# Kernel tuning notes

Measured on AMD Instinct MI355X. Metric: run time of the kernel, lower is better.

The kernel has to match this reference:

```python
import jax, jax.numpy as jnp
import numpy as np

B, S, D = 4, 4096, 1024
E, I = 8, 2048
CAPACITY = 2
K = max(1, int(S / E * CAPACITY))  # tokens per expert per batch element


def setup_inputs() -> dict:
    key = jax.random.key(0)
    k1, k2, k3, k4, k5 = jax.random.split(key, 5)
    x = jax.random.normal(k1, (B, S, D), dtype=jnp.float32)
    gate_w = jax.random.normal(k2, (D, E), dtype=jnp.float32) * 0.006
    Wg = jax.random.normal(k3, (E, D, I), dtype=jnp.float32) * 0.02
    Wu = jax.random.normal(k4, (E, D, I), dtype=jnp.float32) * 0.02
    Wd = jax.random.normal(k5, (E, I, D), dtype=jnp.float32) * 0.02
    return {"x": x, "gate_w": gate_w, "Wg": Wg, "Wu": Wu, "Wd": Wd}


def reference(x, gate_w, Wg, Wu, Wd):
    # Router: softmax over experts per token, then per-expert top-k tokens.
    logits = jnp.einsum('bsd,de->bse', x, gate_w)          # [B,S,E]
    affinity = jax.nn.softmax(logits, axis=-1)
    affinity_T = jnp.transpose(affinity, (0, 2, 1))        # [B,E,S]
    gating, index = jax.lax.top_k(affinity_T, K)           # [B,E,K]

    # Gather selected tokens for all experts at once: [B,E,K,D]
    b_idx = jnp.arange(x.shape[0])[:, None, None]
    x_sel = x[b_idx, index]

    # Per-expert SwiGLU MLP (grouped GEMMs over the expert axis).
    g = jnp.einsum('bekd,edi->beki', x_sel, Wg)
    u = jnp.einsum('bekd,edi->beki', x_sel, Wu)
    h = jax.nn.silu(g) * u
    out = jnp.einsum('beki,eid->bekd', h, Wd)              # [B,E,K,D]

    # Weighted scatter-add combine back to token positions.
    contrib = out * gating[..., None]
    x_out = jnp.zeros_like(x).at[b_idx, index].add(contrib)
    return x_out
```

## Files before the change

kernel.cpp:

```cpp
#include <hip/hip_runtime.h>

#define B_ 4
#define S_ 4096
#define D_ 1024
#define E_ 8
#define I_ 2048
#define K_ 1024

typedef __attribute__((ext_vector_type(8))) short short8;
typedef __attribute__((ext_vector_type(4))) float f32x4;

__device__ __forceinline__ short f2bf(float f) {
  union { float f; unsigned u; } v; v.f = f;
  unsigned r = v.u + 0x7FFFu + ((v.u >> 16) & 1u);
  return (short)(r >> 16);
}

__device__ __forceinline__ void gload16(const void* g, void* l) {
  __builtin_amdgcn_global_load_lds((const __attribute__((address_space(1))) unsigned int*)g,
                                   (__attribute__((address_space(3))) unsigned int*)l, 16, 0, 0);
}

__device__ __forceinline__ short8 rdswz(const short* ls, int row, int cb) {
  int byte = (row << 7) + (cb ^ ((row & 7) << 4));
  return *reinterpret_cast<const short8*>(reinterpret_cast<const char*>(ls) + byte);
}

__global__ __launch_bounds__(256) void router_kernel(const float* __restrict__ x,
                                                     const float* __restrict__ gw,
                                                     double* __restrict__ affD) {
  int wave = threadIdx.x >> 6, lane = threadIdx.x & 63;
  int tok = blockIdx.x * 4 + wave;
  int b = tok >> 12, s = tok & (S_ - 1);
  const float* xr = x + (size_t)tok * D_;
  double acc[E_];
#pragma unroll
  for (int e = 0; e < E_; ++e) acc[e] = 0.0;
#pragma unroll 4
  for (int r = 0; r < 16; ++r) {
    int d = r * 64 + lane;
    float xv = xr[d];
    const float4* g4 = reinterpret_cast<const float4*>(gw + (size_t)d * E_);
    float4 g0 = g4[0], g1 = g4[1];
    acc[0] += (double)xv * g0.x; acc[1] += (double)xv * g0.y;
    acc[2] += (double)xv * g0.z; acc[3] += (double)xv * g0.w;
    acc[4] += (double)xv * g1.x; acc[5] += (double)xv * g1.y;
    acc[6] += (double)xv * g1.z; acc[7] += (double)xv * g1.w;
  }
#pragma unroll
  for (int off = 32; off > 0; off >>= 1) {
#pragma unroll
    for (int e = 0; e < E_; ++e) acc[e] += __shfl_xor(acc[e], off, 64);
  }
  double m = acc[0];
#pragma unroll
  for (int e = 1; e < E_; ++e) m = acc[e] > m ? acc[e] : m;
  double den = 0.0, ex[E_];
#pragma unroll
  for (int e = 0; e < E_; ++e) { ex[e] = exp(acc[e] - m); den += ex[e]; }
  if (lane < E_)
    affD[((size_t)b * E_ + lane) * S_ + s] = ex[lane] / den;
}

__global__ __launch_bounds__(1024) void topk_select_kernel(const double* __restrict__ affD,
                                                           int* __restrict__ idxArr,
                                                           float* __restrict__ gateArr) {
  __shared__ unsigned hist[256];
  __shared__ unsigned s_digit;
  __shared__ int s_rem;
  __shared__ unsigned s_cnt;
  int be = blockIdx.x, tid = threadIdx.x;
  const double* a = affD + (size_t)be * S_;
  unsigned long long key[4];
  bool active[4];
#pragma unroll
  for (int c = 0; c < 4; ++c) {
    int i = tid + c * 1024;
    unsigned long long kb = (unsigned long long)__double_as_longlong(a[i]);
    key[c] = (kb & ~0xFFFULL) | (unsigned long long)(4095 - i);
    active[c] = true;
  }
  int remk = K_;
  unsigned long long prefix = 0;
  for (int pass = 0; pass < 8; ++pass) {
    int shift = 56 - pass * 8;
    if (tid < 256) hist[tid] = 0;
    __syncthreads();
#pragma unroll
    for (int c = 0; c < 4; ++c)
      if (active[c]) atomicAdd(&hist[(unsigned)((key[c] >> shift) & 0xFF)], 1u);
    __syncthreads();
    if (tid == 0) {
      unsigned cum = 0; int d = 255;
      for (; d > 0; --d) {
        unsigned h = hist[d];
        if (cum + h >= (unsigned)remk) break;
        cum += h;
      }
      s_digit = (unsigned)d;
      s_rem = remk - (int)cum;
    }
    __syncthreads();
    unsigned dg = s_digit; remk = s_rem;
    prefix |= ((unsigned long long)dg) << shift;
#pragma unroll
    for (int c = 0; c < 4; ++c)
      active[c] = active[c] && (((key[c] >> shift) & 0xFF) == dg);
    __syncthreads();
  }
  if (tid == 0) s_cnt = 0;
  __syncthreads();
#pragma unroll
  for (int c = 0; c < 4; ++c) {
    if (key[c] >= prefix) {
      unsigned slot = atomicAdd(&s_cnt, 1u);
      int i = 4095 - (int)(key[c] & 0xFFF);
      idxArr[(size_t)be * K_ + slot] = i;
      gateArr[(size_t)be * K_ + slot] = (float)a[i];
    }
  }
}

__global__ __launch_bounds__(256) void transpose_cvt_kernel(const float* __restrict__ in,
                                                            unsigned short* __restrict__ out,
                                                            int M, int N) {
  __shared__ float t[64][65];
  int e = blockIdx.y;
  int ntn = N >> 6;
  int tm = (blockIdx.x / ntn) << 6;
  int tn = (blockIdx.x % ntn) << 6;
  const float* src = in + (size_t)e * M * N;
  unsigned short* dst = out + (size_t)e * M * N;
  int tid = threadIdx.x;
#pragma unroll
  for (int it = 0; it < 4; ++it) {
    int f = it * 256 + tid;
    int r = f >> 4, c4 = (f & 15) << 2;
    float4 v = *reinterpret_cast<const float4*>(&src[(size_t)(tm + r) * N + tn + c4]);
    t[c4][r] = v.x; t[c4 + 1][r] = v.y; t[c4 + 2][r] = v.z; t[c4 + 3][r] = v.w;
  }
  __syncthreads();
#pragma unroll
  for (int it = 0; it < 4; ++it) {
    int f = it * 256 + tid;
    int rr = f >> 4, c4 = (f & 15) << 2;
    short4 o;
    o.x = f2bf(t[rr][c4]); o.y = f2bf(t[rr][c4 + 1]);
    o.z = f2bf(t[rr][c4 + 2]); o.w = f2bf(t[rr][c4 + 3]);
    *reinterpret_cast<short4*>(&dst[(size_t)(tn + rr) * M + tm + c4]) = o;
  }
}

__global__ __launch_bounds__(256) void gather_cvt_kernel(const float* __restrict__ x,
                                                         const int* __restrict__ idxArr,
                                                         unsigned short* __restrict__ Xsel) {
  int row = blockIdx.x * 4 + (threadIdx.x >> 6);
  int lane = threadIdx.x & 63;
  int b = row >> 13;
  int tok = idxArr[row];
  const float* src = x + ((size_t)b * S_ + tok) * D_;
  unsigned short* dst = Xsel + (size_t)row * D_;
#pragma unroll
  for (int it = 0; it < 4; ++it) {
    int d = it * 256 + lane * 4;
    float4 v = *reinterpret_cast<const float4*>(src + d);
    short4 o;
    o.x = f2bf(v.x); o.y = f2bf(v.y); o.z = f2bf(v.z); o.w = f2bf(v.w);
    *reinterpret_cast<short4*>(dst + d) = o;
  }
}

__global__ __launch_bounds__(256, 2) void mlp1_kernel(
    const unsigned short* __restrict__ Xsel, const unsigned short* __restrict__ WgT,
    const unsigned short* __restrict__ WuT, unsigned short* __restrict__ H,
    int Ic, int i0) {
  const int Nt = Ic >> 7;
  int nwg = gridDim.x;
  int bid = (blockIdx.x & 7) * (nwg >> 3) + (blockIdx.x >> 3);
  int nt = bid % Nt; bid /= Nt;
  int mt = bid & 7; bid >>= 3;
  int be = bid;
  int e = be & 7;

  __shared__ short lsA[128 * 64];
  __shared__ short lsBg[128 * 64];
  __shared__ short lsBu[128 * 64];

  int tid = threadIdx.x, w = tid >> 6, lane = tid & 63;
  int wm = w >> 1, wn = w & 1;
  int lr = lane & 15, lg = lane >> 4;

  int srow = lane >> 3;
  int scol = ((lane & 7) ^ srow) << 4;

  const char* pa = (const char*)(Xsel + ((size_t)be * K_ + mt * 128) * D_);
  const char* pg = (const char*)(WgT + (size_t)e * I_ * D_ + (size_t)(i0 + nt * 128) * D_);
  const char* pu = (const char*)(WuT + (size_t)e * I_ * D_ + (size_t)(i0 + nt * 128) * D_);

  f32x4 accg[4][4], accu[4][4];
#pragma unroll
  for (int i = 0; i < 4; ++i)
#pragma unroll
    for (int j = 0; j < 4; ++j) {
      accg[i][j] = (f32x4){0.f, 0.f, 0.f, 0.f};
      accu[i][j] = (f32x4){0.f, 0.f, 0.f, 0.f};
    }

  for (int k0 = 0; k0 < D_; k0 += 64) {
#pragma unroll
    for (int c = 0; c < 4; ++c) {
      int chunk = c * 4 + w;
      int row = chunk * 8 + srow;
      size_t go = (size_t)row * (D_ * 2) + (size_t)k0 * 2 + scol;
      gload16(pa + go, (char*)lsA + chunk * 1024);
      gload16(pg + go, (char*)lsBg + chunk * 1024);
      gload16(pu + go, (char*)lsBu + chunk * 1024);
    }
    __syncthreads();
#pragma unroll
    for (int fk = 0; fk < 2; ++fk) {
      int cb = fk * 64 + lg * 16;
      short8 af[4], bgf[4], buf[4];
#pragma unroll
      for (int fm = 0; fm < 4; ++fm)
        af[fm] = rdswz(lsA, wm * 64 + fm * 16 + lr, cb);
#pragma unroll
      for (int fn = 0; fn < 4; ++fn) {
        bgf[fn] = rdswz(lsBg, wn * 64 + fn * 16 + lr, cb);
        buf[fn] = rdswz(lsBu, wn * 64 + fn * 16 + lr, cb);
      }
#pragma unroll
      for (int fm = 0; fm < 4; ++fm)
#pragma unroll
        for (int fn = 0; fn < 4; ++fn) {
          accg[fm][fn] = __builtin_amdgcn_mfma_f32_16x16x32_bf16(af[fm], bgf[fn], accg[fm][fn], 0, 0, 0);
          accu[fm][fn] = __builtin_amdgcn_mfma_f32_16x16x32_bf16(af[fm], buf[fn], accu[fm][fn], 0, 0, 0);
        }
    }
    __syncthreads();
  }
  unsigned short* Hbe = H + (size_t)be * K_ * Ic;
#pragma unroll
  for (int fm = 0; fm < 4; ++fm)
#pragma unroll
    for (int fn = 0; fn < 4; ++fn) {
#pragma unroll
      for (int j = 0; j < 4; ++j) {
        float g = accg[fm][fn][j], u = accu[fm][fn][j];
        float h = g / (1.f + __expf(-g)) * u;
        int row = wm * 64 + fm * 16 + lg * 4 + j;
        int col = wn * 64 + fn * 16 + lr;
        Hbe[(size_t)(mt * 128 + row) * Ic + nt * 128 + col] = (unsigned short)f2bf(h);
      }
    }
}

__global__ __launch_bounds__(256, 2) void mlp2_kernel(
    const unsigned short* __restrict__ H, const unsigned short* __restrict__ WdT,
    const int* __restrict__ idxArr, const float* __restrict__ gateArr,
    float* __restrict__ out, int Ic, int i0) {
  int nwg = gridDim.x;
  int bid = (blockIdx.x & 7) * (nwg >> 3) + (blockIdx.x >> 3);
  int nt = bid & 7; bid >>= 3;
  int mt = bid & 7; bid >>= 3;
  int be = bid;
  int b = be >> 3, e = be & 7;

  __shared__ short lsA[128 * 64];
  __shared__ short lsB[128 * 64];
  __shared__ int sTok[128];
  __shared__ float sGate[128];

  int tid = threadIdx.x;
  if (tid < 128) {
    sTok[tid] = idxArr[(size_t)be * K_ + mt * 128 + tid];
    sGate[tid] = gateArr[(size_t)be * K_ + mt * 128 + tid];
  }

  const char* pa = (const char*)(H + ((size_t)be * K_ + mt * 128) * Ic);
  const char* pb = (const char*)(WdT + (size_t)e * D_ * I_ + (size_t)(nt * 128) * I_ + i0);

  int w = tid >> 6, lane = tid & 63;
  int wm = w >> 1, wn = w & 1;
  int lr = lane & 15, lg = lane >> 4;

  int srow = lane >> 3;
  int scol = ((lane & 7) ^ srow) << 4;

  f32x4 acc[4][4];
#pragma unroll
  for (int i = 0; i < 4; ++i)
#pragma unroll
    for (int j = 0; j < 4; ++j) acc[i][j] = (f32x4){0.f, 0.f, 0.f, 0.f};

  for (int k0 = 0; k0 < Ic; k0 += 64) {
#pragma unroll
    for (int c = 0; c < 4; ++c) {
      int chunk = c * 4 + w;
      int row = chunk * 8 + srow;
      gload16(pa + (size_t)row * (Ic * 2) + (size_t)k0 * 2 + scol, (char*)lsA + chunk * 1024);
      gload16(pb + (size_t)row * (I_ * 2) + (size_t)k0 * 2 + scol, (char*)lsB + chunk * 1024);
    }
    __syncthreads();
#pragma unroll
    for (int fk = 0; fk < 2; ++fk) {
      int cb = fk * 64 + lg * 16;
      short8 af[4], bf[4];
#pragma unroll
      for (int fm = 0; fm < 4; ++fm)
        af[fm] = rdswz(lsA, wm * 64 + fm * 16 + lr, cb);
#pragma unroll
      for (int fn = 0; fn < 4; ++fn)
        bf[fn] = rdswz(lsB, wn * 64 + fn * 16 + lr, cb);
#pragma unroll
      for (int fm = 0; fm < 4; ++fm)
#pragma unroll
        for (int fn = 0; fn < 4; ++fn)
          acc[fm][fn] = __builtin_amdgcn_mfma_f32_16x16x32_bf16(af[fm], bf[fn], acc[fm][fn], 0, 0, 0);
    }
    __syncthreads();
  }
#pragma unroll
  for (int fm = 0; fm < 4; ++fm)
#pragma unroll
    for (int fn = 0; fn < 4; ++fn) {
#pragma unroll
      for (int j = 0; j < 4; ++j) {
        int row = wm * 64 + fm * 16 + lg * 4 + j;
        int col = nt * 128 + wn * 64 + fn * 16 + lr;
        float v = acc[fm][fn][j] * sGate[row];
        atomicAdd(&out[((size_t)b * S_ + sTok[row]) * D_ + col], v);
      }
    }
}

extern "C" void kernel_launch(void* const* d_in, const int* in_sizes, int n_in,
                              void* d_out, int out_size, void* d_ws, size_t ws_size,
                              hipStream_t stream) {
  const float* x  = (const float*)d_in[0];
  const float* gw = (const float*)d_in[1];
  const float* Wg = (const float*)d_in[2];
  const float* Wu = (const float*)d_in[3];
  const float* Wd = (const float*)d_in[4];
  float* out = (float*)d_out;
  char* ws = (char*)d_ws;

  size_t off = 0;
  double* affD = (double*)(ws + off); off += (size_t)B_ * E_ * S_ * sizeof(double);
  int* idxArr = (int*)(ws + off);     off += (size_t)B_ * E_ * K_ * sizeof(int);
  float* gateArr = (float*)(ws + off); off += (size_t)B_ * E_ * K_ * sizeof(float);
  off = (off + 255) & ~(size_t)255;
  unsigned short* WgT = (unsigned short*)(ws + off); off += (size_t)E_ * D_ * I_ * 2;
  unsigned short* WuT = (unsigned short*)(ws + off); off += (size_t)E_ * D_ * I_ * 2;
  unsigned short* WdT = (unsigned short*)(ws + off); off += (size_t)E_ * D_ * I_ * 2;
  unsigned short* Xsel = (unsigned short*)(ws + off); off += (size_t)B_ * E_ * K_ * D_ * 2;
  off = (off + 255) & ~(size_t)255;
  unsigned short* H = (unsigned short*)(ws + off);
  size_t rem = (ws_size > off) ? (ws_size - off) : 0;

  int Ic = 128;
  for (int c = I_; c >= 128; c >>= 1) {
    if ((size_t)B_ * E_ * K_ * (size_t)c * 2 <= rem) { Ic = c; break; }
  }

  hipMemsetAsync(d_out, 0, (size_t)out_size * sizeof(float), stream);
  router_kernel<<<B_ * S_ / 4, 256, 0, stream>>>(x, gw, affD);
  topk_select_kernel<<<B_ * E_, 1024, 0, stream>>>(affD, idxArr, gateArr);
  transpose_cvt_kernel<<<dim3((D_ / 64) * (I_ / 64), E_), 256, 0, stream>>>(Wg, WgT, D_, I_);
  transpose_cvt_kernel<<<dim3((D_ / 64) * (I_ / 64), E_), 256, 0, stream>>>(Wu, WuT, D_, I_);
  transpose_cvt_kernel<<<dim3((I_ / 64) * (D_ / 64), E_), 256, 0, stream>>>(Wd, WdT, I_, D_);
  gather_cvt_kernel<<<B_ * E_ * K_ / 4, 256, 0, stream>>>(x, idxArr, Xsel);
  for (int i0 = 0; i0 < I_; i0 += Ic) {
    mlp1_kernel<<<B_ * E_ * 8 * (Ic / 128), 256, 0, stream>>>(Xsel, WgT, WuT, H, Ic, i0);
    mlp2_kernel<<<B_ * E_ * 8 * 8, 256, 0, stream>>>(H, WdT, idxArr, gateArr, out, Ic, i0);
  }
}
```

Baseline: 792.6 us.

## Enlarge MLP GEMM tiles to 256x256 with double-buffered LDS pipeline

Both grouped GEMM kernels move to 512-thread blocks with 256x256 (mlp2) or 256x128 interleaved gate/up (mlp1) output tiles. Each kernel now uses 128-wide K stages with double-buffered LDS, prefetching stage t+2 while computing stage t, and raises MFMA priority with setprio. mlp1 packs gate and up rows into a single B tile so one MFMA loop covers both, and SwiGLU is applied across paired fragments. The aim is more data reuse per loaded byte and overlap of global loads with compute, at the cost of larger LDS and register use, which may lower occupancy.

```diff
diff --git a/kernel.cpp b/kernel.cpp
--- a/kernel.cpp
+++ b/kernel.cpp
@@ -170,7 +170,7 @@
   }
 }
 
-__global__ __launch_bounds__(256, 2) void mlp1_kernel(
+__global__ __launch_bounds__(512, 2) void mlp1_kernel(
     const unsigned short* __restrict__ Xsel, const unsigned short* __restrict__ WgT,
     const unsigned short* __restrict__ WuT, unsigned short* __restrict__ H,
     int Ic, int i0) {
@@ -178,156 +178,203 @@
   int nwg = gridDim.x;
   int bid = (blockIdx.x & 7) * (nwg >> 3) + (blockIdx.x >> 3);
   int nt = bid % Nt; bid /= Nt;
-  int mt = bid & 7; bid >>= 3;
+  int mt = bid & 3; bid >>= 2;
   int be = bid;
   int e = be & 7;
 
-  __shared__ short lsA[128 * 64];
-  __shared__ short lsBg[128 * 64];
-  __shared__ short lsBu[128 * 64];
+  __shared__ short lsA[2][256 * 64];
+  __shared__ short lsB[2][256 * 64];
 
   int tid = threadIdx.x, w = tid >> 6, lane = tid & 63;
-  int wm = w >> 1, wn = w & 1;
+  int wm = w >> 2, wn = w & 3;
   int lr = lane & 15, lg = lane >> 4;
-
   int srow = lane >> 3;
   int scol = ((lane & 7) ^ srow) << 4;
 
-  const char* pa = (const char*)(Xsel + ((size_t)be * K_ + mt * 128) * D_);
-  const char* pg = (const char*)(WgT + (size_t)e * I_ * D_ + (size_t)(i0 + nt * 128) * D_);
-  const char* pu = (const char*)(WuT + (size_t)e * I_ * D_ + (size_t)(i0 + nt * 128) * D_);
-
-  f32x4 accg[4][4], accu[4][4];
-#pragma unroll
-  for (int i = 0; i < 4; ++i)
-#pragma unroll
-    for (int j = 0; j < 4; ++j) {
-      accg[i][j] = (f32x4){0.f, 0.f, 0.f, 0.f};
-      accu[i][j] = (f32x4){0.f, 0.f, 0.f, 0.f};
-    }
-
-  for (int k0 = 0; k0 < D_; k0 += 64) {
-#pragma unroll
-    for (int c = 0; c < 4; ++c) {
-      int chunk = c * 4 + w;
-      int row = chunk * 8 + srow;
-      size_t go = (size_t)row * (D_ * 2) + (size_t)k0 * 2 + scol;
-      gload16(pa + go, (char*)lsA + chunk * 1024);
-      gload16(pg + go, (char*)lsBg + chunk * 1024);
-      gload16(pu + go, (char*)lsBu + chunk * 1024);
-    }
-    __syncthreads();
-#pragma unroll
-    for (int fk = 0; fk < 2; ++fk) {
-      int cb = fk * 64 + lg * 16;
-      short8 af[4], bgf[4], buf[4];
-#pragma unroll
-      for (int fm = 0; fm < 4; ++fm)
-        af[fm] = rdswz(lsA, wm * 64 + fm * 16 + lr, cb);
-#pragma unroll
-      for (int fn = 0; fn < 4; ++fn) {
-        bgf[fn] = rdswz(lsBg, wn * 64 + fn * 16 + lr, cb);
-        buf[fn] = rdswz(lsBu, wn * 64 + fn * 16 + lr, cb);
+  const char* pa = (const char*)(Xsel + ((size_t)be * K_ + mt * 256) * D_);
+  const char* pg = (const char*)(WgT + ((size_t)e * I_ + i0 + nt * 128) * D_);
+  const char* pu = (const char*)(WuT + ((size_t)e * I_ + i0 + nt * 128) * D_);
+
+  auto STAGE = [&](int t) {
+    int buf = t & 1;
+    int kb = t * 128;
+#pragma unroll
+    for (int ch = 0; ch < 4; ++ch) {
+      int rb = ch * 64 + w * 8;
+      int r = rb + srow;
+      gload16(pa + (size_t)r * 2048 + kb + scol, (char*)(&lsA[buf][0]) + rb * 128);
+      int hu = (r >> 4) & 1;
+      int iloc = ((r >> 5) << 4) + (r & 15);
+      const char* pb = hu ? pu : pg;
+      gload16(pb + (size_t)iloc * 2048 + kb + scol, (char*)(&lsB[buf][0]) + rb * 128);
+    }
+  };
+
+  f32x4 acc[8][4];
+#pragma unroll
+  for (int i = 0; i < 8; ++i)
+#pragma unroll
+    for (int j = 0; j < 4; ++j) acc[i][j] = (f32x4){0.f, 0.f, 0.f, 0.f};
+
+  const int NT = 16;
+  STAGE(0);
+  STAGE(1);
+  asm volatile("s_waitcnt vmcnt(8) lgkmcnt(0)" ::: "memory");
+  __builtin_amdgcn_s_barrier();
+
+  for (int t = 0; t < NT; ++t) {
+    const short* A = &lsA[t & 1][0];
+    const short* Bt = &lsB[t & 1][0];
+    short8 af0[8], bf0[4];
+#pragma unroll
+    for (int fm = 0; fm < 8; ++fm) af0[fm] = rdswz(A, wm * 128 + fm * 16 + lr, lg * 16);
+#pragma unroll
+    for (int fn = 0; fn < 4; ++fn) bf0[fn] = rdswz(Bt, wn * 64 + fn * 16 + lr, lg * 16);
+    __builtin_amdgcn_s_setprio(1);
+#pragma unroll
+    for (int fm = 0; fm < 8; ++fm)
+#pragma unroll
+      for (int fn = 0; fn < 4; ++fn)
+        acc[fm][fn] = __builtin_amdgcn_mfma_f32_16x16x32_bf16(af0[fm], bf0[fn], acc[fm][fn], 0, 0, 0);
+    __builtin_amdgcn_s_setprio(0);
+    short8 af1[8], bf1[4];
+#pragma unroll
+    for (int fm = 0; fm < 8; ++fm) af1[fm] = rdswz(A, wm * 128 + fm * 16 + lr, 64 + lg * 16);
+#pragma unroll
+    for (int fn = 0; fn < 4; ++fn) bf1[fn] = rdswz(Bt, wn * 64 + fn * 16 + lr, 64 + lg * 16);
+    asm volatile("s_waitcnt lgkmcnt(0)" ::: "memory");
+    __builtin_amdgcn_s_barrier();
+    if (t + 2 < NT) STAGE(t + 2);
+    __builtin_amdgcn_s_setprio(1);
+#pragma unroll
+    for (int fm = 0; fm < 8; ++fm)
+#pragma unroll
+      for (int fn = 0; fn < 4; ++fn)
+        acc[fm][fn] = __builtin_amdgcn_mfma_f32_16x16x32_bf16(af1[fm], bf1[fn], acc[fm][fn], 0, 0, 0);
+    __builtin_amdgcn_s_setprio(0);
+    if (t + 1 < NT) {
+      if (t + 2 < NT) asm volatile("s_waitcnt vmcnt(8)" ::: "memory");
+      else            asm volatile("s_waitcnt vmcnt(0)" ::: "memory");
+      __builtin_amdgcn_s_barrier();
+    }
+  }
+
+  unsigned short* Hbe = H + (size_t)be * K_ * Ic;
+#pragma unroll
+  for (int fm = 0; fm < 8; ++fm)
+#pragma unroll
+    for (int q = 0; q < 2; ++q)
+#pragma unroll
+      for (int j = 0; j < 4; ++j) {
+        float g = acc[fm][2 * q][j], u = acc[fm][2 * q + 1][j];
+        float h = g / (1.f + __expf(-g)) * u;
+        int row = mt * 256 + wm * 128 + fm * 16 + lg * 4 + j;
+        int col = nt * 128 + (wn * 2 + q) * 16 + lr;
+        Hbe[(size_t)row * Ic + col] = (unsigned short)f2bf(h);
       }
-#pragma unroll
-      for (int fm = 0; fm < 4; ++fm)
-#pragma unroll
-        for (int fn = 0; fn < 4; ++fn) {
-          accg[fm][fn] = __builtin_amdgcn_mfma_f32_16x16x32_bf16(af[fm], bgf[fn], accg[fm][fn], 0, 0, 0);
-          accu[fm][fn] = __builtin_amdgcn_mfma_f32_16x16x32_bf16(af[fm], buf[fn], accu[fm][fn], 0, 0, 0);
-        }
-    }
-    __syncthreads();
-  }
-  unsigned short* Hbe = H + (size_t)be * K_ * Ic;
-#pragma unroll
-  for (int fm = 0; fm < 4; ++fm)
-#pragma unroll
-    for (int fn = 0; fn < 4; ++fn) {
-#pragma unroll
-      for (int j = 0; j < 4; ++j) {
-        float g = accg[fm][fn][j], u = accu[fm][fn][j];
-        float h = g / (1.f + __expf(-g)) * u;
-        int row = wm * 64 + fm * 16 + lg * 4 + j;
-        int col = wn * 64 + fn * 16 + lr;
-        Hbe[(size_t)(mt * 128 + row) * Ic + nt * 128 + col] = (unsigned short)f2bf(h);
-      }
-    }
-}
-
-__global__ __launch_bounds__(256, 2) void mlp2_kernel(
+}
+
+__global__ __launch_bounds__(512, 2) void mlp2_kernel(
     const unsigned short* __restrict__ H, const unsigned short* __restrict__ WdT,
     const int* __restrict__ idxArr, const float* __restrict__ gateArr,
     float* __restrict__ out, int Ic, int i0) {
   int nwg = gridDim.x;
   int bid = (blockIdx.x & 7) * (nwg >> 3) + (blockIdx.x >> 3);
-  int nt = bid & 7; bid >>= 3;
-  int mt = bid & 7; bid >>= 3;
+  int nt = bid & 3; bid >>= 2;
+  int mt = bid & 3; bid >>= 2;
   int be = bid;
   int b = be >> 3, e = be & 7;
 
-  __shared__ short lsA[128 * 64];
-  __shared__ short lsB[128 * 64];
-  __shared__ int sTok[128];
-  __shared__ float sGate[128];
-
-  int tid = threadIdx.x;
-  if (tid < 128) {
-    sTok[tid] = idxArr[(size_t)be * K_ + mt * 128 + tid];
-    sGate[tid] = gateArr[(size_t)be * K_ + mt * 128 + tid];
-  }
-
-  const char* pa = (const char*)(H + ((size_t)be * K_ + mt * 128) * Ic);
-  const char* pb = (const char*)(WdT + (size_t)e * D_ * I_ + (size_t)(nt * 128) * I_ + i0);
-
-  int w = tid >> 6, lane = tid & 63;
-  int wm = w >> 1, wn = w & 1;
+  __shared__ short lsA[2][256 * 64];
+  __shared__ short lsB[2][256 * 64];
+  __shared__ int sTok[256];
+  __shared__ float sGate[256];
+
+  int tid = threadIdx.x, w = tid >> 6, lane = tid & 63;
+  int wm = w >> 2, wn = w & 3;
   int lr = lane & 15, lg = lane >> 4;
-
   int srow = lane >> 3;
   int scol = ((lane & 7) ^ srow) << 4;
 
-  f32x4 acc[4][4];
-#pragma unroll
-  for (int i = 0; i < 4; ++i)
+  if (tid < 256) {
+    size_t gbase = (size_t)be * K_ + mt * 256 + tid;
+    sTok[tid] = idxArr[gbase];
+    sGate[tid] = gateArr[gbase];
+  }
+
+  const char* pa = (const char*)(H + ((size_t)be * K_ + mt * 256) * Ic);
+  const char* pb = (const char*)(WdT + ((size_t)e * D_ + nt * 256) * I_ + i0);
+  size_t strideA = (size_t)Ic * 2;
+
+  auto STAGE = [&](int t) {
+    int buf = t & 1;
+    int kb = t * 128;
+#pragma unroll
+    for (int ch = 0; ch < 4; ++ch) {
+      int rb = ch * 64 + w * 8;
+      int r = rb + srow;
+      gload16(pa + (size_t)r * strideA + kb + scol, (char*)(&lsA[buf][0]) + rb * 128);
+      gload16(pb + (size_t)r * 4096 + kb + scol, (char*)(&lsB[buf][0]) + rb * 128);
+    }
+  };
+
+  f32x4 acc[8][4];
+#pragma unroll
+  for (int i = 0; i < 8; ++i)
 #pragma unroll
     for (int j = 0; j < 4; ++j) acc[i][j] = (f32x4){0.f, 0.f, 0.f, 0.f};
 
-  for (int k0 = 0; k0 < Ic; k0 += 64) {
-#pragma unroll
-    for (int c = 0; c < 4; ++c) {
-      int chunk = c * 4 + w;
-      int row = chunk * 8 + srow;
-      gload16(pa + (size_t)row * (Ic * 2) + (size_t)k0 * 2 + scol, (char*)lsA + chunk * 1024);
-      gload16(pb + (size_t)row * (I_ * 2) + (size_t)k0 * 2 + scol, (char*)lsB + chunk * 1024);
-    }
-    __syncthreads();
-#pragma unroll
-    for (int fk = 0; fk < 2; ++fk) {
-      int cb = fk * 64 + lg * 16;
-      short8 af[4], bf[4];
-#pragma unroll
-      for (int fm = 0; fm < 4; ++fm)
-        af[fm] = rdswz(lsA, wm * 64 + fm * 16 + lr, cb);
+  const int NT = Ic >> 6;
+  STAGE(0);
+  STAGE(1);
+  asm volatile("s_waitcnt vmcnt(8) lgkmcnt(0)" ::: "memory");
+  __builtin_amdgcn_s_barrier();
+
+  for (int t = 0; t < NT; ++t) {
+    const short* A = &lsA[t & 1][0];
+    const short* Bt = &lsB[t & 1][0];
+    short8 af0[8], bf0[4];
+#pragma unroll
+    for (int fm = 0; fm < 8; ++fm) af0[fm] = rdswz(A, wm * 128 + fm * 16 + lr, lg * 16);
+#pragma unroll
+    for (int fn = 0; fn < 4; ++fn) bf0[fn] = rdswz(Bt, wn * 64 + fn * 16 + lr, lg * 16);
+    __builtin_amdgcn_s_setprio(1);
+#pragma unroll
+    for (int fm = 0; fm < 8; ++fm)
 #pragma unroll
       for (int fn = 0; fn < 4; ++fn)
-        bf[fn] = rdswz(lsB, wn * 64 + fn * 16 + lr, cb);
-#pragma unroll
-      for (int fm = 0; fm < 4; ++fm)
-#pragma unroll
-        for (int fn = 0; fn < 4; ++fn)
-          acc[fm][fn] = __builtin_amdgcn_mfma_f32_16x16x32_bf16(af[fm], bf[fn], acc[fm][fn], 0, 0, 0);
-    }
-    __syncthreads();
-  }
-#pragma unroll
-  for (int fm = 0; fm < 4; ++fm)
+        acc[fm][fn] = __builtin_amdgcn_mfma_f32_16x16x32_bf16(af0[fm], bf0[fn], acc[fm][fn], 0, 0, 0);
+    __builtin_amdgcn_s_setprio(0);
+    short8 af1[8], bf1[4];
+#pragma unroll
+    for (int fm = 0; fm < 8; ++fm) af1[fm] = rdswz(A, wm * 128 + fm * 16 + lr, 64 + lg * 16);
+#pragma unroll
+    for (int fn = 0; fn < 4; ++fn) bf1[fn] = rdswz(Bt, wn * 64 + fn * 16 + lr, 64 + lg * 16);
+    asm volatile("s_waitcnt lgkmcnt(0)" ::: "memory");
+    __builtin_amdgcn_s_barrier();
+    if (t + 2 < NT) STAGE(t + 2);
+    __builtin_amdgcn_s_setprio(1);
+#pragma unroll
+    for (int fm = 0; fm < 8; ++fm)
+#pragma unroll
+      for (int fn = 0; fn < 4; ++fn)
+        acc[fm][fn] = __builtin_amdgcn_mfma_f32_16x16x32_bf16(af1[fm], bf1[fn], acc[fm][fn], 0, 0, 0);
+    __builtin_amdgcn_s_setprio(0);
+    if (t + 1 < NT) {
+      if (t + 2 < NT) asm volatile("s_waitcnt vmcnt(8)" ::: "memory");
+      else            asm volatile("s_waitcnt vmcnt(0)" ::: "memory");
+      __builtin_amdgcn_s_barrier();
+    }
+  }
+
+#pragma unroll
+  for (int fm = 0; fm < 8; ++fm)
 #pragma unroll
     for (int fn = 0; fn < 4; ++fn) {
 #pragma unroll
       for (int j = 0; j < 4; ++j) {
-        int row = wm * 64 + fm * 16 + lg * 4 + j;
-        int col = nt * 128 + wn * 64 + fn * 16 + lr;
+        int row = wm * 128 + fm * 16 + lg * 4 + j;
+        int col = nt * 256 + wn * 64 + fn * 16 + lr;
         float v = acc[fm][fn][j] * sGate[row];
         atomicAdd(&out[((size_t)b * S_ + sTok[row]) * D_ + col], v);
       }
@@ -371,7 +418,7 @@
   transpose_cvt_kernel<<<dim3((I_ / 64) * (D_ / 64), E_), 256, 0, stream>>>(Wd, WdT, I_, D_);
   gather_cvt_kernel<<<B_ * E_ * K_ / 4, 256, 0, stream>>>(x, idxArr, Xsel);
   for (int i0 = 0; i0 < I_; i0 += Ic) {
-    mlp1_kernel<<<B_ * E_ * 8 * (Ic / 128), 256, 0, stream>>>(Xsel, WgT, WuT, H, Ic, i0);
-    mlp2_kernel<<<B_ * E_ * 8 * 8, 256, 0, stream>>>(H, WdT, idxArr, gateArr, out, Ic, i0);
-  }
-}
+    mlp1_kernel<<<B_ * E_ * 4 * (Ic / 128), 512, 0, stream>>>(Xsel, WgT, WuT, H, Ic, i0);
+    mlp2_kernel<<<B_ * E_ * 4 * 4, 512, 0, stream>>>(H, WdT, idxArr, gateArr, out, Ic, i0);
+  }
+}
```

After: 834.2 us. 1.05x slower.
